# Optimization experiments

Hardware: AMD Instinct MI355X
Metric: run time of the kernel (lower is better)

## Reference

```python
import jax, jax.numpy as jnp
import numpy as np

H = 1024   # LSTM hidden (hardcoded in init_states)
A = 128    # attention / speaker dim
M = 80     # mel channels
TXT = 512  # text embedding dim
E = TXT + A
V = 185    # Flowtron symbol vocab
T = 512    # mel frames
TT = 192   # text tokens
SCALE = 0.05


def setup_inputs() -> dict:
    key = jax.random.key(0)
    ks = jax.random.split(key, 24)
    def rn(k, shape, s=SCALE):
        return jax.random.normal(k, shape, jnp.float32) * s
    return {
        "residual": jax.random.normal(ks[0], (1, M, T), jnp.float32),
        "speaker_vecs": jax.random.normal(ks[1], (1, A), jnp.float32),
        "emb": rn(ks[2], (V, TXT), 1.0),
        "Wih_att": rn(ks[3], (2, 4 * H, M)),
        "Whh_att": rn(ks[4], (2, 4 * H, H)),
        "b_att": jnp.zeros((2, 4 * H), jnp.float32),
        "Wq": rn(ks[5], (2, H, A)),
        "Wk": rn(ks[6], (2, E, A)),
        "Wv": rn(ks[7], (2, E, A)),
        "Wih1": rn(ks[8], (2, 4 * H, H + A)),
        "Whh1": rn(ks[9], (2, 4 * H, H)),
        "b1": jnp.zeros((2, 4 * H), jnp.float32),
        "Wih2": rn(ks[10], (2, 4 * H, H)),
        "Whh2": rn(ks[11], (2, 4 * H, H)),
        "b2": jnp.zeros((2, 4 * H), jnp.float32),
        "Wd": rn(ks[12], (2, H, H)),
        "bd": jnp.zeros((2, H), jnp.float32),
        "Wo": rn(ks[13], (2, H, 2 * M), 0.01),
        "bo": jnp.zeros((2, 2 * M), jnp.float32),
        "Wg": rn(ks[14], (2, H + A, 1)),
        "bg": jnp.zeros((2, 1), jnp.float32),
        "text": jax.random.randint(ks[15], (1, TT), 0, V),
    }


def _cell(x, h, c, Wih, Whh, b):
    # standard LSTM cell, gate order i,f,g,o
    z = x @ Wih.T + h @ Whh.T + b
    i, f, g, o = jnp.split(z, 4, axis=-1)
    c = jax.nn.sigmoid(f) * c + jax.nn.sigmoid(i) * jnp.tanh(g)
    h = jax.nn.sigmoid(o) * jnp.tanh(c)
    return h, c


def _run_flow(seq, enc, p, reverse):
    (Wih_att, Whh_att, b_att, Wq, Wk, Wv, Wih1, Whh1, b1,
     Wih2, Whh2, b2, Wd, bd, Wo, bo, Wg, bg) = p
    keys = enc @ Wk   # [TT, A] precomputed outside the scan
    vals = enc @ Wv   # [TT, A]
    inv = jnp.float32(1.0 / np.sqrt(A))
    def step(carry, x_t):
        prev, ha, ca, h1, c1, h2, c2 = carry
        ha, ca = _cell(prev, ha, ca, Wih_att, Whh_att, b_att)
        attn = jax.nn.softmax((ha @ Wq) @ keys.T * inv, axis=-1)  # [1, TT]
        ctx = attn @ vals                                          # [1, A]
        di = jnp.concatenate([ha, ctx], axis=-1)                   # [1, H+A]
        gate = jax.nn.sigmoid(di @ Wg + bg)  # gate computed; early-exit replaced by full-length scan
        h1, c1 = _cell(di, h1, c1, Wih1, Whh1, b1)
        h2, c2 = _cell(h1, h2, c2, Wih2, Whh2, b2)
        hd = jnp.tanh(h2 @ Wd + bd)
        out = hd @ Wo + bo
        b_p, log_s = jnp.split(out, 2, axis=-1)
        y = (x_t - b_p) * jnp.exp(-log_s)   # inverse affine coupling
        return (y, ha, ca, h1, c1, h2, c2), y
    z0 = jnp.zeros((1, M), seq.dtype)
    zh = jnp.zeros((1, H), seq.dtype)
    xs = seq[::-1] if reverse else seq
    _, ys = jax.lax.scan(step, (z0, zh, zh, zh, zh, zh, zh), xs)  # ys: [T, 1, M]
    return ys[::-1] if reverse else ys


def reference(residual, speaker_vecs, emb, Wih_att, Whh_att, b_att, Wq, Wk, Wv,
              Wih1, Whh1, b1, Wih2, Whh2, b2, Wd, bd, Wo, bo, Wg, bg, text):
    # encoder: text embedding concat broadcast speaker vector -> [TT, E]
    enc = jnp.concatenate(
        [emb[text[0]], jnp.broadcast_to(speaker_vecs, (text.shape[1], speaker_vecs.shape[1]))], axis=-1)
    stacked = (Wih_att, Whh_att, b_att, Wq, Wk, Wv, Wih1, Whh1, b1,
               Wih2, Whh2, b2, Wd, bd, Wo, bo, Wg, bg)
    seq = jnp.transpose(residual, (2, 0, 1))   # [T, 1, M]
    seq = _run_flow(seq, enc, tuple(w[1] for w in stacked), reverse=True)   # backward flow
    seq = _run_flow(seq, enc, tuple(w[0] for w in stacked), reverse=False)  # forward flow
    return jnp.transpose(seq, (1, 2, 0))       # [1, M, T]
```

## Files before the change

### kernel.cpp

```cpp
#include <hip/hip_runtime.h>
#include <hip/hip_bf16.h>
#include <stdint.h>

#define AG __HIP_MEMORY_SCOPE_AGENT
typedef unsigned long long ull;

static constexpr size_t OFF_WA  = 0;
static constexpr size_t OFF_W1  = 18874368;
static constexpr size_t OFF_W2  = 54657024;
static constexpr size_t OFF_WD  = 88342528;
static constexpr size_t OFF_WO  = 92536832;
static constexpr size_t OFF_WQ  = 93192192;
static constexpr size_t OFF_VL  = 93978624;
static constexpr size_t OFF_KEY = 94109696;
static constexpr size_t OFF_V32 = 94306304;
static constexpr size_t OFF_WQT = 94502912;
static constexpr size_t OFF_ENC = 95551488;
static constexpr size_t OFF_RB  = 96043008;
static constexpr size_t OFF_SEQ = 96206848;
static constexpr size_t OFF_DYN = 96370688;
static constexpr size_t OFF_HAb = OFF_DYN + 0;
static constexpr size_t OFF_H1b = OFF_DYN + 4096;
static constexpr size_t OFF_H2b = OFF_DYN + 8192;
static constexpr size_t OFF_HDb = OFF_DYN + 12288;
static constexpr size_t OFF_YBb = OFF_DYN + 16384;
static constexpr size_t OFF_SCb = OFF_DYN + 16896;
static constexpr size_t DYN_BYTES = 18432;
static constexpr size_t NEEDED = OFF_DYN + DYN_BYTES;

__device__ __forceinline__ float aldx(const float* p){ return __hip_atomic_load(p, __ATOMIC_RELAXED, AG); }
__device__ __forceinline__ void  astx(float* p, float v){ __hip_atomic_store(p, v, __ATOMIC_RELAXED, AG); }
__device__ __forceinline__ int   PADI(int k){ return k + ((k>>5)<<2); }
__device__ __forceinline__ float tagf(float f, uint32_t tag){
  return __uint_as_float((__float_as_uint(f) & ~3u) | tag);
}

__device__ __forceinline__ float dot8(uint4 w, const float* v){
  float4 a = *(const float4*)v;
  float4 b = *(const float4*)(v+4);
  float s;
  s = __uint_as_float(w.x << 16) * a.x;
  s = fmaf(__uint_as_float(w.x & 0xffff0000u), a.y, s);
  s = fmaf(__uint_as_float(w.y << 16),         a.z, s);
  s = fmaf(__uint_as_float(w.y & 0xffff0000u), a.w, s);
  s = fmaf(__uint_as_float(w.z << 16),         b.x, s);
  s = fmaf(__uint_as_float(w.z & 0xffff0000u), b.y, s);
  s = fmaf(__uint_as_float(w.w << 16),         b.z, s);
  s = fmaf(__uint_as_float(w.w & 0xffff0000u), b.w, s);
  return s;
}
__device__ __forceinline__ float dot4(uint2 w, const float* v){
  float4 a = *(const float4*)v;
  float s;
  s = __uint_as_float(w.x << 16) * a.x;
  s = fmaf(__uint_as_float(w.x & 0xffff0000u), a.y, s);
  s = fmaf(__uint_as_float(w.y << 16),         a.z, s);
  s = fmaf(__uint_as_float(w.y & 0xffff0000u), a.w, s);
  return s;
}
__device__ __forceinline__ float sigf(float x){ return 1.f/(1.f+__expf(-x)); }
__device__ __forceinline__ float tanhf_(float x){
  x = fminf(12.f, fmaxf(-12.f, x));
  float t = __expf(2.f*x);
  return (t-1.f)/(t+1.f);
}

__global__ void k_init(float* z, int n){ int i = blockIdx.x*256 + threadIdx.x; if (i<n) z[i]=0.f; }

__global__ void k_rbuf(const float* res, float* rb){
  int i = blockIdx.x*256 + threadIdx.x; if (i >= 512*80) return;
  int t = i/80, m = i - t*80;
  rb[i] = res[m*512 + t];
}

__global__ void k_enc(const float* emb, const float* spk, const int* text, float* enc){
  int i = blockIdx.x*256 + threadIdx.x; if (i >= 192*640) return;
  int s = i/640, e = i - s*640;
  enc[i] = (e < 512) ? emb[(size_t)text[s]*512 + e] : spk[e-512];
}

__global__ void k_keysvals(const float* enc, const float* Wk, const float* Wv,
                           float* keys, float* vals32){
  int i = blockIdx.x*256 + threadIdx.x; if (i >= 2*192*128) return;
  int f = i/(192*128); int r = i - f*192*128; int s = r/128, a = r - s*128;
  float ka=0.f, va=0.f;
  for (int e=0;e<640;++e){
    float x = enc[s*640+e];
    ka = fmaf(x, Wk[((size_t)f*640+e)*128+a], ka);
    va = fmaf(x, Wv[((size_t)f*640+e)*128+a], va);
  }
  keys[((size_t)f*192+s)*128+a] = ka;
  vals32[((size_t)f*192+s)*128+a] = va;
}

__global__ void k_wqT(const float* Wq, float* WqT){
  int i = blockIdx.x*256 + threadIdx.x; if (i >= 2*128*1024) return;
  int f = i/(128*1024); int r = i - f*128*1024; int a = r/1024, h = r - a*1024;
  WqT[i] = Wq[((size_t)f*1024+h)*128+a];
}

__global__ void k_wqk2(const float* WqT, const float* keys, uint2* dst){
  int b = blockIdx.x; int f = b/192, s = b - f*192;
  int t = threadIdx.x;
  float4 acc = {0.f,0.f,0.f,0.f};
  const float* kp = keys + ((size_t)f*192+s)*128;
  const float* wp = WqT + (size_t)f*128*1024 + t*4;
  for (int a=0;a<128;++a){
    float kk = kp[a];
    float4 w = *(const float4*)(wp + (size_t)a*1024);
    acc.x = fmaf(kk, w.x, acc.x); acc.y = fmaf(kk, w.y, acc.y);
    acc.z = fmaf(kk, w.z, acc.z); acc.w = fmaf(kk, w.w, acc.w);
  }
  const float inv = 0.08838834764831845f;
  __hip_bfloat16 b0 = __float2bfloat16(acc.x*inv), b1 = __float2bfloat16(acc.y*inv);
  __hip_bfloat16 b2 = __float2bfloat16(acc.z*inv), b3 = __float2bfloat16(acc.w*inv);
  uint2 o;
  o.x = (uint32_t)(*(uint16_t*)&b0) | ((uint32_t)(*(uint16_t*)&b1) << 16);
  o.y = (uint32_t)(*(uint16_t*)&b2) | ((uint32_t)(*(uint16_t*)&b3) << 16);
  dst[((size_t)f*192+s)*256 + t] = o;
}

__device__ __forceinline__ uint32_t pk2(float a, float b){
  __hip_bfloat16 x = __float2bfloat16(a), y = __float2bfloat16(b);
  return (uint32_t)(*(uint16_t*)&x) | ((uint32_t)(*(uint16_t*)&y) << 16);
}

__global__ void k_packV2(const float* vals32, uint4* dst){
  int i = blockIdx.x*256 + threadIdx.x; if (i >= 2*192*16) return;
  int ag = i & 15; int r = i >> 4;
  int s = r % 192; int f = r / 192;
  float v[8];
  for (int e=0;e<8;++e) v[e] = vals32[((size_t)f*192+s)*128 + ag*8 + e];
  uint4 o; o.x = pk2(v[0],v[1]); o.y = pk2(v[2],v[3]); o.z = pk2(v[4],v[5]); o.w = pk2(v[6],v[7]);
  dst[i] = o;
}

__global__ void k_packA2(const float* Wih, const float* Whh, uint4* dst){
  int i = blockIdx.x*256 + threadIdx.x; if (i >= 2*256*256*9) return;
  int j = i % 9; int r = i / 9;
  int t = r & 255; r >>= 8;
  int b = r & 255; int f = r >> 8;
  int rs = t>>4, ks = t&15;
  int row = (rs>>2)*1024 + b*4 + (rs&3);
  float v[8];
  for (int e=0;e<8;++e){
    int c = ks*8 + e;
    if (j == 0) v[e] = (c < 80) ? Wih[((size_t)f*4096+row)*80 + c] : 0.f;
    else        v[e] = Whh[((size_t)f*4096+row)*1024 + (j-1)*128 + c];
  }
  uint4 o; o.x = pk2(v[0],v[1]); o.y = pk2(v[2],v[3]); o.z = pk2(v[4],v[5]); o.w = pk2(v[6],v[7]);
  dst[i] = o;
}

__global__ void k_pack1b(const float* Wih1, const float* Whh1, uint4* dst){
  int i = blockIdx.x*256 + threadIdx.x; if (i >= 2*256*16*273) return;
  int kc = i % 273; int r = i / 273;
  int rr = r & 15; r >>= 4;
  int b = r & 255; int f = r >> 8;
  int row = (rr>>2)*1024 + b*4 + (rr&3);
  int k0 = kc*8;
  float v[8];
  for (int e=0;e<8;++e){
    int k = k0+e; float x;
    if (k < 1024)      x = Wih1[((size_t)f*4096+row)*1152 + k];
    else if (k < 2048) x = Whh1[((size_t)f*4096+row)*1024 + (k-1024)];
    else if (k < 2176) x = Wih1[((size_t)f*4096+row)*1152 + 1024 + (k-2048)];
    else               x = 0.f;
    v[e] = x;
  }
  uint4 o; o.x = pk2(v[0],v[1]); o.y = pk2(v[2],v[3]); o.z = pk2(v[4],v[5]); o.w = pk2(v[6],v[7]);
  dst[i] = o;
}

__global__ void k_pack2b(const float* Wih2, const float* Whh2, uint4* dst){
  int i = blockIdx.x*256 + threadIdx.x; if (i >= 2*256*16*257) return;
  int kc = i % 257; int r = i / 257;
  int rr = r & 15; r >>= 4;
  int b = r & 255; int f = r >> 8;
  int row = (rr>>2)*1024 + b*4 + (rr&3);
  int k0 = kc*8;
  float v[8];
  for (int e=0;e<8;++e){
    int k = k0+e;
    v[e] = (k < 1024) ? Wih2[((size_t)f*4096+row)*1024 + k]
         : (k < 2048) ? Whh2[((size_t)f*4096+row)*1024 + (k-1024)] : 0.f;
  }
  uint4 o; o.x = pk2(v[0],v[1]); o.y = pk2(v[2],v[3]); o.z = pk2(v[4],v[5]); o.w = pk2(v[6],v[7]);
  dst[i] = o;
}

__global__ void k_packD2(const float* Wd, uint4* dst){
  __shared__ float tile[64][65];
  int b = blockIdx.x; int f = b >> 8; int rem = b & 255;
  int ot = rem >> 4, ct = rem & 15;
  int tid = threadIdx.x;
  for (int i = tid; i < 4096; i += 256){
    int rc = i >> 6, oc = i & 63;
    tile[rc][oc] = Wd[((size_t)f*1024 + ct*64 + rc)*1024 + ot*64 + oc];
  }
  __syncthreads();
  for (int w = 0; w < 2; ++w){
    int idx = w*256 + tid;
    int op = idx >> 3, cc = idx & 7;
    int k6 = (ct&7)*8 + cc, j = ct >> 3;
    int o = ot*64 + op;
    int b2 = o >> 2, r2 = o & 3;
    uint4 out;
    out.x = pk2(tile[cc*8+0][op], tile[cc*8+1][op]);
    out.y = pk2(tile[cc*8+2][op], tile[cc*8+3][op]);
    out.z = pk2(tile[cc*8+4][op], tile[cc*8+5][op]);
    out.w = pk2(tile[cc*8+6][op], tile[cc*8+7][op]);
    dst[((((size_t)f*256 + b2)*256) + r2*64 + k6)*2 + j] = out;
  }
}

__global__ void k_packO2(const float* Wo, uint2* dst){
  int i = blockIdx.x*256 + threadIdx.x; if (i >= 2*80*256) return;
  int t = i & 255; int r = i >> 8;
  int m = r % 80; int f = r / 80;
  for (int j = 0; j < 2; ++j){
    int row = m + j*80;
    float v[4];
    for (int e=0;e<4;++e) v[e] = Wo[((size_t)f*1024 + t*4+e)*160 + row];
    uint2 o; o.x = pk2(v[0],v[1]); o.y = pk2(v[2],v[3]);
    dst[(size_t)i*2 + j] = o;
  }
}

__launch_bounds__(256, 1)
__global__ void k_flow8(uint8_t* ws, int fl, int rev, int out_mode, int hot,
    const float* b_att_all, const float* b1_all, const float* b2_all,
    const float* bd_all, const float* bo_all,
    const float* xsrc, float* ydst)
{
  const int tid = threadIdx.x, bid = blockIdx.x;
  const int rs = tid >> 4, ks = tid & 15;
  const int wid = tid >> 6;
  const int ko = ks*8 + ((ks>>2)<<2);

  float* habuf = (float*)(ws + OFF_HAb);
  float* h1buf = (float*)(ws + OFF_H1b);
  float* h2buf = (float*)(ws + OFF_H2b);
  float* hdbuf = (float*)(ws + OFF_HDb);
  float* ybuf  = (float*)(ws + OFF_YBb);
  float* scb   = (float*)(ws + OFF_SCb);

  __shared__ __align__(16) ushort W1s[16*2184];
  __shared__ __align__(16) ushort W2s[16*2056];
  __shared__ __align__(16) float haPrevS[1152];
  __shared__ __align__(16) float S2[1152];
  __shared__ __align__(16) float S3[1152];
  __shared__ __align__(16) float scratch[2048];
  __shared__ __align__(16) float yS[144];
  __shared__ __align__(16) float ctxS[144];
  __shared__ __align__(16) float attp[288];
  __shared__ float zred[32];
  __shared__ float cst[3][4];
  __shared__ float bAs[16], b1s[16], b2s[16], bds[4], bos[2];

  const size_t fb = (size_t)fl*256 + bid;

  { const uint4* src = (const uint4*)((const ushort*)(ws + OFF_W1) + fb*16*2184);
    uint4* dst = (uint4*)W1s;
    for (int i = tid; i < 4368; i += 256) dst[i] = src[i]; }
  { const uint4* src = (const uint4*)((const ushort*)(ws + OFF_W2) + fb*16*2056);
    uint4* dst = (uint4*)W2s;
    for (int i = tid; i < 4112; i += 256) dst[i] = src[i]; }
  uint4 wa[9];
  { const uint4* g = (const uint4*)(ws + OFF_WA) + (fb*256 + tid)*9;
    #pragma unroll
    for (int j = 0; j < 9; ++j) wa[j] = g[j]; }
  uint4 wd[2];
  { const uint4* g = (const uint4*)(ws + OFF_WD) + (fb*256 + tid)*2;
    wd[0] = g[0]; wd[1] = g[1]; }
  uint2 wqk = {0,0};
  if (bid < 192) wqk = ((const uint2*)(ws + OFF_WQ))[((size_t)fl*192 + bid)*256 + tid];
  uint4 vals_r[12];
  { const uint4* g = (const uint4*)(ws + OFF_VL) + (((size_t)fl*192 + rs*12)*16 + ks);
    #pragma unroll
    for (int j = 0; j < 12; ++j) vals_r[j] = g[(size_t)j*16]; }
  uint2 wo0 = {0,0}, wo1 = {0,0};
  if (bid < 80){ const uint2* g = (const uint2*)(ws + OFF_WO) + (((size_t)fl*80 + bid)*256 + tid)*2;
    wo0 = g[0]; wo1 = g[1]; }
  if (tid < 16){
    int g = tid >> 2, uu = tid & 3;
    bAs[tid] = b_att_all[fl*4096 + g*1024 + bid*4 + uu];
    b1s[tid] = b1_all  [fl*4096 + g*1024 + bid*4 + uu];
    b2s[tid] = b2_all  [fl*4096 + g*1024 + bid*4 + uu];
  }
  if (tid < 4)  bds[tid] = bd_all[fl*1024 + bid*4 + tid];
  if (tid < 2 && bid < 80) bos[tid] = bo_all[fl*160 + tid*80 + bid];
  if (tid < 12) ((float*)cst)[tid] = 0.f;
  for (int i = tid; i < 1152; i += 256){ haPrevS[i]=0.f; S2[i]=0.f; S3[i]=0.f; }
  if (tid < 144){ yS[tid]=0.f; ctxS[tid]=0.f; }
  __syncthreads();

  auto poll4 = [&](const float* g, float* s, uint32_t tag){
    float v0,v1,v2,v3;
    for(;;){
      v0 = aldx(g+tid);     v1 = aldx(g+tid+256);
      v2 = aldx(g+tid+512); v3 = aldx(g+tid+768);
      uint32_t ok = ((__float_as_uint(v0)&3u)==tag) & ((__float_as_uint(v1)&3u)==tag)
                  & ((__float_as_uint(v2)&3u)==tag) & ((__float_as_uint(v3)&3u)==tag);
      if (ok) break;
      if (!hot) __builtin_amdgcn_s_sleep(1);
    }
    s[PADI(tid)]     = v0;  s[PADI(tid+256)] = v1;
    s[PADI(tid+512)] = v2;  s[PADI(tid+768)] = v3;
  };
  auto poll1 = [&](const float* g, int n, float* s, uint32_t tag){
    if (tid < n){
      float f;
      for(;;){ f = aldx(g+tid); if((__float_as_uint(f)&3u)==tag) break;
               if (!hot) __builtin_amdgcn_s_sleep(1); }
      s[PADI(tid)] = f;
    }
  };

  const uint4* w1row = (const uint4*)(W1s) + (size_t)rs*273;
  const uint4* w2row = (const uint4*)(W2s) + (size_t)rs*257;

  float accA = 0.f;

  for (int t = 0; t < 512; ++t) {
    const int col = rev ? (511 - t) : t;
    const uint32_t TAG = (uint32_t)((t+1) & 3);
    float x = 0.f;
    if (bid < 80) x = xsrc[col*80 + bid];

    {
      float acc = accA + dot8(wa[0], yS + ko);
      acc += __shfl_xor(acc,1); acc += __shfl_xor(acc,2);
      acc += __shfl_xor(acc,4); acc += __shfl_xor(acc,8);
      if (ks == 0) zred[rs] = acc + bAs[rs];
    }
    __syncthreads();
    if (tid < 4) {
      float zi=zred[tid], zf=zred[4+tid], zg=zred[8+tid], zo=zred[12+tid];
      float c = sigf(zf)*cst[0][tid] + sigf(zi)*tanhf_(zg);
      float h = sigf(zo)*tanhf_(c);
      cst[0][tid] = c;
      astx(habuf + bid*4 + tid, tagf(h, TAG));
    }

    float acc1 = 0.f, acc2 = 0.f;
    #pragma unroll
    for (int j = 0; j < 8; ++j) acc1 += dot8(w1row[(j+8)*16 + ks], S2 + j*144 + ko);
    #pragma unroll
    for (int j = 0; j < 8; ++j) acc2 += dot8(w2row[(j+8)*16 + ks], S3 + j*144 + ko);

    poll4(habuf, haPrevS, TAG);
    __syncthreads();

    if (bid < 192) {
      float sv = dot4(wqk, haPrevS + tid*4 + ((tid>>3)<<2));
      #pragma unroll
      for (int d=1; d<64; d<<=1) sv += __shfl_xor(sv, d);
      if ((tid&63) == 0) zred[16+wid] = sv;
      __syncthreads();
      if (tid == 0) astx(scb + bid, tagf(zred[16]+zred[17]+zred[18]+zred[19], TAG));
    }

    #pragma unroll
    for (int j = 0; j < 8; ++j) acc1 += dot8(w1row[j*16 + ks], haPrevS + j*144 + ko);

    poll1(scb, 192, attp, TAG);
    __syncthreads();

    {
      float v = (tid < 192) ? attp[PADI(tid)] : -3.0e38f;
      float m = v;
      #pragma unroll
      for (int d=1; d<64; d<<=1) m = fmaxf(m, __shfl_xor(m, d));
      if ((tid&63) == 0) zred[16+wid] = m;
      __syncthreads();
      float mx = fmaxf(fmaxf(zred[16],zred[17]), fmaxf(zred[18],zred[19]));
      float e = (tid < 192) ? __expf(v - mx) : 0.f;
      float sm = e;
      #pragma unroll
      for (int d=1; d<64; d<<=1) sm += __shfl_xor(sm, d);
      if ((tid&63) == 0) zred[20+wid] = sm;
      __syncthreads();
      float inv = 1.f / (zred[20]+zred[21]+zred[22]+zred[23]);
      attp[PADI(tid)] = (tid < 192) ? e * inv : 0.f;
    }
    __syncthreads();
    {
      float pc0=0,pc1=0,pc2=0,pc3=0,pc4=0,pc5=0,pc6=0,pc7=0;
      #pragma unroll
      for (int j = 0; j < 12; ++j){
        float pj = attp[PADI(rs*12 + j)];
        uint4 v = vals_r[j];
        pc0 = fmaf(__uint_as_float(v.x << 16),         pj, pc0);
        pc1 = fmaf(__uint_as_float(v.x & 0xffff0000u), pj, pc1);
        pc2 = fmaf(__uint_as_float(v.y << 16),         pj, pc2);
        pc3 = fmaf(__uint_as_float(v.y & 0xffff0000u), pj, pc3);
        pc4 = fmaf(__uint_as_float(v.z << 16),         pj, pc4);
        pc5 = fmaf(__uint_as_float(v.z & 0xffff0000u), pj, pc5);
        pc6 = fmaf(__uint_as_float(v.w << 16),         pj, pc6);
        pc7 = fmaf(__uint_as_float(v.w & 0xffff0000u), pj, pc7);
      }
      *(float4*)&scratch[tid*8]   = make_float4(pc0,pc1,pc2,pc3);
      *(float4*)&scratch[tid*8+4] = make_float4(pc4,pc5,pc6,pc7);
    }
    __syncthreads();
    if (tid < 128){
      float s = 0.f;
      #pragma unroll
      for (int sg = 0; sg < 16; ++sg) s += scratch[sg*128 + tid];
      ctxS[PADI(tid)] = s;
    }
    __syncthreads();

    {
      acc1 += dot8(w1row[256 + ks], ctxS + ko);
      acc1 += __shfl_xor(acc1,1); acc1 += __shfl_xor(acc1,2);
      acc1 += __shfl_xor(acc1,4); acc1 += __shfl_xor(acc1,8);
      if (ks == 0) zred[rs] = acc1 + b1s[rs];
    }
    __syncthreads();
    if (tid < 4) {
      float zi=zred[tid], zf=zred[4+tid], zg=zred[8+tid], zo=zred[12+tid];
      float c = sigf(zf)*cst[1][tid] + sigf(zi)*tanhf_(zg);
      float h = sigf(zo)*tanhf_(c);
      cst[1][tid] = c;
      astx(h1buf + bid*4 + tid, tagf(h, TAG));
    }

    {
      float a = 0.f;
      #pragma unroll
      for (int j = 1; j < 9; ++j) a += dot8(wa[j], haPrevS + (j-1)*144 + ko);
      accA = a;
    }

    poll4(h1buf, S2, TAG);
    __syncthreads();

    {
      #pragma unroll
      for (int j = 0; j < 8; ++j) acc2 += dot8(w2row[j*16 + ks], S2 + j*144 + ko);
      acc2 += __shfl_xor(acc2,1); acc2 += __shfl_xor(acc2,2);
      acc2 += __shfl_xor(acc2,4); acc2 += __shfl_xor(acc2,8);
      if (ks == 0) zred[rs] = acc2 + b2s[rs];
    }
    __syncthreads();
    if (tid < 4) {
      float zi=zred[tid], zf=zred[4+tid], zg=zred[8+tid], zo=zred[12+tid];
      float c = sigf(zf)*cst[2][tid] + sigf(zi)*tanhf_(zg);
      float h = sigf(zo)*tanhf_(c);
      cst[2][tid] = c;
      astx(h2buf + bid*4 + tid, tagf(h, TAG));
    }

    poll4(h2buf, S3, TAG);
    __syncthreads();

    {
      int k6 = tid & 63, r2 = tid >> 6;
      int kk = k6*8 + ((k6>>2)<<2);
      float acc = dot8(wd[0], S3 + kk) + dot8(wd[1], S3 + 576 + kk);
      #pragma unroll
      for (int d=1; d<64; d<<=1) acc += __shfl_xor(acc, d);
      if (k6 == 0) astx(hdbuf + bid*4 + r2, tagf(tanhf_(acc + bds[r2]), TAG));
    }

    if (bid < 80) {
      poll4(hdbuf, scratch, TAG);
      __syncthreads();
      int po = tid*4 + ((tid>>3)<<2);
      float pb = dot4(wo0, scratch + po);
      float pl = dot4(wo1, scratch + po);
      #pragma unroll
      for (int d=1; d<64; d<<=1) { pb += __shfl_xor(pb, d); pl += __shfl_xor(pl, d); }
      if ((tid & 63) == 0) { zred[16+wid] = pb; zred[20+wid] = pl; }
      __syncthreads();
      if (tid == 0) {
        float bp = zred[16]+zred[17]+zred[18]+zred[19] + bos[0];
        float ls = zred[20]+zred[21]+zred[22]+zred[23] + bos[1];
        float y = (x - bp) * __expf(-ls);
        if (out_mode == 0) ydst[col*80 + bid] = y;
        else               ydst[bid*512 + col] = y;
        astx(ybuf + bid, tagf(y, TAG));
      }
    }

    poll1(ybuf, 80, yS, TAG);
    __syncthreads();
  }
}

extern "C" void kernel_launch(void* const* d_in, const int* in_sizes, int n_in,
                              void* d_out, int out_size, void* d_ws, size_t ws_size,
                              hipStream_t stream) {
  if (ws_size < NEEDED) return;
  uint8_t* ws = (uint8_t*)d_ws;
  const float* residual = (const float*)d_in[0];
  const float* spk      = (const float*)d_in[1];
  const float* emb      = (const float*)d_in[2];
  const float* Wih_att  = (const float*)d_in[3];
  const float* Whh_att  = (const float*)d_in[4];
  const float* b_att    = (const float*)d_in[5];
  const float* Wq       = (const float*)d_in[6];
  const float* Wk       = (const float*)d_in[7];
  const float* Wv       = (const float*)d_in[8];
  const float* Wih1     = (const float*)d_in[9];
  const float* Whh1     = (const float*)d_in[10];
  const float* b1       = (const float*)d_in[11];
  const float* Wih2     = (const float*)d_in[12];
  const float* Whh2     = (const float*)d_in[13];
  const float* b2       = (const float*)d_in[14];
  const float* Wd       = (const float*)d_in[15];
  const float* bd       = (const float*)d_in[16];
  const float* Wo       = (const float*)d_in[17];
  const float* bo       = (const float*)d_in[18];
  const int*   text     = (const int*)d_in[21];

  dim3 B(256);
  k_rbuf<<<160, B, 0, stream>>>(residual, (float*)(ws+OFF_RB));
  k_enc<<<480, B, 0, stream>>>(emb, spk, text, (float*)(ws+OFF_ENC));
  k_keysvals<<<192, B, 0, stream>>>((const float*)(ws+OFF_ENC), Wk, Wv,
                                    (float*)(ws+OFF_KEY), (float*)(ws+OFF_V32));
  k_wqT<<<1024, B, 0, stream>>>(Wq, (float*)(ws+OFF_WQT));
  k_wqk2<<<384, B, 0, stream>>>((const float*)(ws+OFF_WQT), (const float*)(ws+OFF_KEY),
                                (uint2*)(ws+OFF_WQ));
  k_packV2<<<24, B, 0, stream>>>((const float*)(ws+OFF_V32), (uint4*)(ws+OFF_VL));
  k_packA2<<<4608, B, 0, stream>>>(Wih_att, Whh_att, (uint4*)(ws+OFF_WA));
  k_pack1b<<<8736, B, 0, stream>>>(Wih1, Whh1, (uint4*)(ws+OFF_W1));
  k_pack2b<<<8224, B, 0, stream>>>(Wih2, Whh2, (uint4*)(ws+OFF_W2));
  k_packD2<<<512, B, 0, stream>>>(Wd, (uint4*)(ws+OFF_WD));
  k_packO2<<<160, B, 0, stream>>>(Wo, (uint2*)(ws+OFF_WO));

  k_init<<<18, B, 0, stream>>>((float*)(ws+OFF_DYN), (int)(DYN_BYTES/4));
  k_flow8<<<256, B, 0, stream>>>(ws, 1, 1, 0, 1, b_att, b1, b2, bd, bo,
                                 (const float*)(ws+OFF_RB), (float*)(ws+OFF_SEQ));
  k_init<<<18, B, 0, stream>>>((float*)(ws+OFF_DYN), (int)(DYN_BYTES/4));
  k_flow8<<<256, B, 0, stream>>>(ws, 0, 0, 1, 0, b_att, b1, b2, bd, bo,
                                 (const float*)(ws+OFF_SEQ), (float*)d_out);
}
```

Baseline: 26.39 ms.

## Publish coupling params instead of y, fuse softmax into one wave, drop poll sleeps

Output blocks now publish the tagged bias and log-scale values, not the final y. Every block rebuilds y locally from a preloaded x row, so the x load moves off the critical path. The attention-score softmax now runs in a single wavefront that polls the scores directly, with scores spaced four floats apart to avoid sharing cache lines, which removes several block-wide barriers. Sleep backoff in the spin loops is removed for both flows, which adds polling traffic, and each block now recomputes a few exponentials per step.

```diff
diff --git a/kernel.cpp b/kernel.cpp
--- a/kernel.cpp
+++ b/kernel.cpp
@@ -23,9 +23,9 @@
 static constexpr size_t OFF_H1b = OFF_DYN + 4096;
 static constexpr size_t OFF_H2b = OFF_DYN + 8192;
 static constexpr size_t OFF_HDb = OFF_DYN + 12288;
-static constexpr size_t OFF_YBb = OFF_DYN + 16384;
-static constexpr size_t OFF_SCb = OFF_DYN + 16896;
-static constexpr size_t DYN_BYTES = 18432;
+static constexpr size_t OFF_BPL = OFF_DYN + 16384;
+static constexpr size_t OFF_SCb = OFF_DYN + 17408;
+static constexpr size_t DYN_BYTES = 20480;
 static constexpr size_t NEEDED = OFF_DYN + DYN_BYTES;
 
 __device__ __forceinline__ float aldx(const float* p){ return __hip_atomic_load(p, __ATOMIC_RELAXED, AG); }
@@ -47,6 +47,18 @@
   s = fmaf(__uint_as_float(w.z & 0xffff0000u), b.y, s);
   s = fmaf(__uint_as_float(w.w << 16),         b.z, s);
   s = fmaf(__uint_as_float(w.w & 0xffff0000u), b.w, s);
+  return s;
+}
+__device__ __forceinline__ float dot8r(uint4 w, const float* y){
+  float s;
+  s = __uint_as_float(w.x << 16) * y[0];
+  s = fmaf(__uint_as_float(w.x & 0xffff0000u), y[1], s);
+  s = fmaf(__uint_as_float(w.y << 16),         y[2], s);
+  s = fmaf(__uint_as_float(w.y & 0xffff0000u), y[3], s);
+  s = fmaf(__uint_as_float(w.z << 16),         y[4], s);
+  s = fmaf(__uint_as_float(w.z & 0xffff0000u), y[5], s);
+  s = fmaf(__uint_as_float(w.w << 16),         y[6], s);
+  s = fmaf(__uint_as_float(w.w & 0xffff0000u), y[7], s);
   return s;
 }
 __device__ __forceinline__ float dot4(uint2 w, const float* v){
@@ -228,7 +240,7 @@
 }
 
 __launch_bounds__(256, 1)
-__global__ void k_flow8(uint8_t* ws, int fl, int rev, int out_mode, int hot,
+__global__ void k_flow9(uint8_t* ws, int fl, int rev, int out_mode,
     const float* b_att_all, const float* b1_all, const float* b2_all,
     const float* bd_all, const float* bo_all,
     const float* xsrc, float* ydst)
@@ -242,7 +254,7 @@
   float* h1buf = (float*)(ws + OFF_H1b);
   float* h2buf = (float*)(ws + OFF_H2b);
   float* hdbuf = (float*)(ws + OFF_HDb);
-  float* ybuf  = (float*)(ws + OFF_YBb);
+  float* bpl   = (float*)(ws + OFF_BPL);
   float* scb   = (float*)(ws + OFF_SCb);
 
   __shared__ __align__(16) ushort W1s[16*2184];
@@ -251,9 +263,10 @@
   __shared__ __align__(16) float S2[1152];
   __shared__ __align__(16) float S3[1152];
   __shared__ __align__(16) float scratch[2048];
-  __shared__ __align__(16) float yS[144];
   __shared__ __align__(16) float ctxS[144];
   __shared__ __align__(16) float attp[288];
+  __shared__ __align__(16) float bplS[184];
+  __shared__ float xrow[80];
   __shared__ float zred[32];
   __shared__ float cst[3][4];
   __shared__ float bAs[16], b1s[16], b2s[16], bds[4], bos[2];
@@ -292,7 +305,8 @@
   if (tid < 2 && bid < 80) bos[tid] = bo_all[fl*160 + tid*80 + bid];
   if (tid < 12) ((float*)cst)[tid] = 0.f;
   for (int i = tid; i < 1152; i += 256){ haPrevS[i]=0.f; S2[i]=0.f; S3[i]=0.f; }
-  if (tid < 144){ yS[tid]=0.f; ctxS[tid]=0.f; }
+  if (tid < 184) bplS[tid] = 0.f;
+  if (tid < 80)  xrow[tid] = 0.f;
   __syncthreads();
 
   auto poll4 = [&](const float* g, float* s, uint32_t tag){
@@ -303,7 +317,6 @@
       uint32_t ok = ((__float_as_uint(v0)&3u)==tag) & ((__float_as_uint(v1)&3u)==tag)
                   & ((__float_as_uint(v2)&3u)==tag) & ((__float_as_uint(v3)&3u)==tag);
       if (ok) break;
-      if (!hot) __builtin_amdgcn_s_sleep(1);
     }
     s[PADI(tid)]     = v0;  s[PADI(tid+256)] = v1;
     s[PADI(tid+512)] = v2;  s[PADI(tid+768)] = v3;
@@ -311,8 +324,7 @@
   auto poll1 = [&](const float* g, int n, float* s, uint32_t tag){
     if (tid < n){
       float f;
-      for(;;){ f = aldx(g+tid); if((__float_as_uint(f)&3u)==tag) break;
-               if (!hot) __builtin_amdgcn_s_sleep(1); }
+      for(;;){ f = aldx(g+tid); if((__float_as_uint(f)&3u)==tag) break; }
       s[PADI(tid)] = f;
     }
   };
@@ -325,11 +337,15 @@
   for (int t = 0; t < 512; ++t) {
     const int col = rev ? (511 - t) : t;
     const uint32_t TAG = (uint32_t)((t+1) & 3);
-    float x = 0.f;
-    if (bid < 80) x = xsrc[col*80 + bid];
 
     {
-      float acc = accA + dot8(wa[0], yS + ko);
+      float yv[8];
+      #pragma unroll
+      for (int e = 0; e < 8; ++e){
+        int k = ks*8 + e;
+        yv[e] = (k < 80) ? (xrow[k] - bplS[PADI(k)]) * __expf(-bplS[PADI(80+k)]) : 0.f;
+      }
+      float acc = accA + dot8r(wa[0], yv);
       acc += __shfl_xor(acc,1); acc += __shfl_xor(acc,2);
       acc += __shfl_xor(acc,4); acc += __shfl_xor(acc,8);
       if (ks == 0) zred[rs] = acc + bAs[rs];
@@ -356,35 +372,38 @@
       float sv = dot4(wqk, haPrevS + tid*4 + ((tid>>3)<<2));
       #pragma unroll
       for (int d=1; d<64; d<<=1) sv += __shfl_xor(sv, d);
+      if (tid == 0){
+      }
       if ((tid&63) == 0) zred[16+wid] = sv;
       __syncthreads();
-      if (tid == 0) astx(scb + bid, tagf(zred[16]+zred[17]+zred[18]+zred[19], TAG));
+      if (tid == 0) astx(scb + bid*4, tagf(zred[16]+zred[17]+zred[18]+zred[19], TAG));
     }
 
     #pragma unroll
     for (int j = 0; j < 8; ++j) acc1 += dot8(w1row[j*16 + ks], haPrevS + j*144 + ko);
 
-    poll1(scb, 192, attp, TAG);
-    __syncthreads();
-
-    {
-      float v = (tid < 192) ? attp[PADI(tid)] : -3.0e38f;
-      float m = v;
+    if (tid < 64){
+      float f0,f1,f2;
+      for(;;){
+        f0 = aldx(scb + tid*4); f1 = aldx(scb + (tid+64)*4); f2 = aldx(scb + (tid+128)*4);
+        uint32_t ok = ((__float_as_uint(f0)&3u)==TAG) & ((__float_as_uint(f1)&3u)==TAG)
+                    & ((__float_as_uint(f2)&3u)==TAG);
+        if (ok) break;
+      }
+      float m = fmaxf(f0, fmaxf(f1, f2));
       #pragma unroll
       for (int d=1; d<64; d<<=1) m = fmaxf(m, __shfl_xor(m, d));
-      if ((tid&63) == 0) zred[16+wid] = m;
-      __syncthreads();
-      float mx = fmaxf(fmaxf(zred[16],zred[17]), fmaxf(zred[18],zred[19]));
-      float e = (tid < 192) ? __expf(v - mx) : 0.f;
-      float sm = e;
+      float e0 = __expf(f0 - m), e1 = __expf(f1 - m), e2 = __expf(f2 - m);
+      float sm = e0 + e1 + e2;
       #pragma unroll
       for (int d=1; d<64; d<<=1) sm += __shfl_xor(sm, d);
-      if ((tid&63) == 0) zred[20+wid] = sm;
-      __syncthreads();
-      float inv = 1.f / (zred[20]+zred[21]+zred[22]+zred[23]);
-      attp[PADI(tid)] = (tid < 192) ? e * inv : 0.f;
-    }
-    __syncthreads();
+      float inv = 1.f / sm;
+      attp[PADI(tid)]     = e0 * inv;
+      attp[PADI(tid+64)]  = e1 * inv;
+      attp[PADI(tid+128)] = e2 * inv;
+    }
+    __syncthreads();
+
     {
       float pc0=0,pc1=0,pc2=0,pc3=0,pc4=0,pc5=0,pc6=0,pc7=0;
       #pragma unroll
@@ -455,6 +474,7 @@
 
     poll4(h2buf, S3, TAG);
     __syncthreads();
+    if (tid < 80) xrow[tid] = xsrc[col*80 + tid];
 
     {
       int k6 = tid & 63, r2 = tid >> 6;
@@ -476,16 +496,17 @@
       if ((tid & 63) == 0) { zred[16+wid] = pb; zred[20+wid] = pl; }
       __syncthreads();
       if (tid == 0) {
-        float bp = zred[16]+zred[17]+zred[18]+zred[19] + bos[0];
-        float ls = zred[20]+zred[21]+zred[22]+zred[23] + bos[1];
-        float y = (x - bp) * __expf(-ls);
+        float bp = tagf(zred[16]+zred[17]+zred[18]+zred[19] + bos[0], TAG);
+        float ls = tagf(zred[20]+zred[21]+zred[22]+zred[23] + bos[1], TAG);
+        astx(bpl + bid, bp);
+        astx(bpl + 80 + bid, ls);
+        float y = (xrow[bid] - bp) * __expf(-ls);
         if (out_mode == 0) ydst[col*80 + bid] = y;
         else               ydst[bid*512 + col] = y;
-        astx(ybuf + bid, tagf(y, TAG));
       }
     }
 
-    poll1(ybuf, 80, yS, TAG);
+    poll1(bpl, 160, bplS, TAG);
     __syncthreads();
   }
 }
@@ -531,10 +552,10 @@
   k_packD2<<<512, B, 0, stream>>>(Wd, (uint4*)(ws+OFF_WD));
   k_packO2<<<160, B, 0, stream>>>(Wo, (uint2*)(ws+OFF_WO));
 
-  k_init<<<18, B, 0, stream>>>((float*)(ws+OFF_DYN), (int)(DYN_BYTES/4));
-  k_flow8<<<256, B, 0, stream>>>(ws, 1, 1, 0, 1, b_att, b1, b2, bd, bo,
+  k_init<<<20, B, 0, stream>>>((float*)(ws+OFF_DYN), (int)(DYN_BYTES/4));
+  k_flow9<<<256, B, 0, stream>>>(ws, 1, 1, 0, b_att, b1, b2, bd, bo,
                                  (const float*)(ws+OFF_RB), (float*)(ws+OFF_SEQ));
-  k_init<<<18, B, 0, stream>>>((float*)(ws+OFF_DYN), (int)(DYN_BYTES/4));
-  k_flow8<<<256, B, 0, stream>>>(ws, 0, 0, 1, 0, b_att, b1, b2, bd, bo,
+  k_init<<<20, B, 0, stream>>>((float*)(ws+OFF_DYN), (int)(DYN_BYTES/4));
+  k_flow9<<<256, B, 0, stream>>>(ws, 0, 0, 1, b_att, b1, b2, bd, bo,
                                  (const float*)(ws+OFF_SEQ), (float*)d_out);
 }
```

After: 27.87 ms. 1.06x slower.
